# Optimization experiments

Measured on AMD Instinct MI355X. Metric: run time of the kernel, lower is better.

## Reference

```python
import jax, jax.numpy as jnp
import numpy as np

CH = 128
GROUPS = 8
HEADS = 8
HEAD_DIM = CH // HEADS  # 16
EPS = 1e-5


def setup_inputs() -> dict:
    key = jax.random.key(0)
    ks = jax.random.split(key, 5)
    x = jax.random.normal(ks[0], (8, CH, 128, 128), dtype=jnp.float32)
    gn_w = jnp.ones((CH,), dtype=jnp.float32)
    gn_b = jnp.zeros((CH,), dtype=jnp.float32)
    w_in = jax.random.normal(ks[1], (CH, CH), dtype=jnp.float32) * (1.0 / np.sqrt(CH))
    b_in = jax.random.normal(ks[2], (CH,), dtype=jnp.float32) * 0.01
    w_out = jax.random.normal(ks[3], (CH, CH), dtype=jnp.float32) * (1.0 / np.sqrt(CH))
    b_out = jax.random.normal(ks[4], (CH,), dtype=jnp.float32) * 0.01
    return {"x": x, "gn_w": gn_w, "gn_b": gn_b, "w_in": w_in, "b_in": b_in,
            "w_out": w_out, "b_out": b_out}


def _group_norm(x, gamma, beta):
    b, c, H, W = x.shape
    xg = x.reshape(b, GROUPS, c // GROUPS, H, W)
    mean = xg.mean(axis=(2, 3, 4), keepdims=True)
    var = xg.var(axis=(2, 3, 4), keepdims=True)
    xg = (xg - mean) * jax.lax.rsqrt(var + EPS)
    x = xg.reshape(b, c, H, W)
    return x * gamma[None, :, None, None] + beta[None, :, None, None]


def _conv1x1(x, w, bias):
    # w: [out_c, in_c] (1x1 conv == pointwise matmul over channels)
    return jnp.einsum('oc,bchw->bohw', w, x) + bias[None, :, None, None]


def reference(x, gn_w, gn_b, w_in, b_in, w_out, b_out):
    b, c, H, W = x.shape
    h = _group_norm(x, gn_w, gn_b)
    h = _conv1x1(h, w_in, b_in)
    # reshape to [b, heads, head_dim, H*W]; attention over head_dim axis,
    # contracting the spatial axis (d = H*W) as in the original einsums
    hh = h.reshape(b, HEADS, HEAD_DIM, H * W)
    scale = HEAD_DIM ** (-0.5)
    scores = jnp.einsum('bhid,bhjd->bhij', hh, hh) * scale  # [b,heads,hd,hd]
    weights = jax.nn.softmax(scores, axis=-1)
    attn = jnp.einsum('bhij,bhjd->bhid', weights, hh)
    attn = attn.reshape(b, c, H, W)
    h = _conv1x1(attn, w_out, b_out)
    return x + h
```

## Files before the change

kernel.cpp:

```cpp
#include <hip/hip_runtime.h>


#define NPOS 16384
#define PITCH 136

typedef short short8 __attribute__((ext_vector_type(8)));
typedef float f32x4 __attribute__((ext_vector_type(4)));

__device__ __forceinline__ unsigned short f2bf(float f) {
    union { float f; unsigned u; } v; v.f = f;
    unsigned r = (v.u + 0x7fffu + ((v.u >> 16) & 1u)) >> 16;
    return (unsigned short)r;
}

__global__ __launch_bounds__(256) void k_stats(const float* __restrict__ x,
                                               float* __restrict__ stats) {
    const float4* p = (const float4*)(x + (size_t)blockIdx.x * 16384);
    int t = threadIdx.x;
    float s1 = 0.f, s2 = 0.f;
#pragma unroll
    for (int j = 0; j < 16; ++j) {
        float4 v = p[t + j * 256];
        s1 += v.x + v.y + v.z + v.w;
        s2 += v.x * v.x + v.y * v.y + v.z * v.z + v.w * v.w;
    }
    for (int off = 32; off; off >>= 1) {
        s1 += __shfl_down(s1, off);
        s2 += __shfl_down(s2, off);
    }
    __shared__ float r1[4], r2[4];
    int wv = t >> 6;
    if ((t & 63) == 0) { r1[wv] = s1; r2[wv] = s2; }
    __syncthreads();
    if (t == 0) {
        s1 = r1[0] + r1[1] + r1[2] + r1[3];
        s2 = r2[0] + r2[1] + r2[2] + r2[3];
        int bg = blockIdx.x >> 4;
        atomicAdd(&stats[bg * 2 + 0], s1);
        atomicAdd(&stats[bg * 2 + 1], s2);
    }
}

__global__ __launch_bounds__(128) void k_prep(const float* __restrict__ stats,
                                              const float* __restrict__ gn_w,
                                              const float* __restrict__ gn_b,
                                              const float* __restrict__ w_in,
                                              const float* __restrict__ b_in,
                                              float* __restrict__ sA,
                                              float* __restrict__ vA) {
    int b = blockIdx.x, c = threadIdx.x;
    int g = c >> 4;
    float s1 = stats[(b * 8 + g) * 2 + 0];
    float s2 = stats[(b * 8 + g) * 2 + 1];
    const float invN = 1.0f / 262144.0f;
    float mean = s1 * invN;
    float var = s2 * invN - mean * mean;
    float rstd = rsqrtf(var + 1e-5f);
    float s = gn_w[c] * rstd;
    float tt = gn_b[c] - mean * s;
    __shared__ float tl[128];
    tl[c] = tt;
    sA[b * 128 + c] = s;
    __syncthreads();
    float v = b_in[c];
    const float* wr = w_in + c * 128;
#pragma unroll 8
    for (int k = 0; k < 128; ++k) v += wr[k] * tl[k];
    vA[b * 128 + c] = v;
}

__global__ __launch_bounds__(256, 2) void k_gemm1_scores(const float* __restrict__ x,
                                                         const float* __restrict__ w_in,
                                                         const float* __restrict__ sA,
                                                         const float* __restrict__ vA,
                                                         float* __restrict__ Sg) {
    __shared__ unsigned short As[128 * PITCH];
    __shared__ unsigned short Xt[128 * PITCH];
    __shared__ float v_s[128];

    const int t = threadIdx.x;
    const int lane = t & 63, wv = t >> 6;
    const int q = lane >> 4, i16 = lane & 15;
    const int b = blockIdx.x >> 7;
    const int p0 = (blockIdx.x & 127) << 7;

    if (t < 128) v_s[t] = vA[b * 128 + t];

    {
        const float4* w4 = (const float4*)w_in;
        const float4* s4 = (const float4*)(sA + b * 128);
#pragma unroll
        for (int i = 0; i < 16; ++i) {
            int idx = t + i * 256;
            int c = idx >> 5, k4 = idx & 31;
            float4 w = w4[idx];
            float4 s = s4[k4];
            ushort4 o;
            o.x = f2bf(w.x * s.x); o.y = f2bf(w.y * s.y);
            o.z = f2bf(w.z * s.z); o.w = f2bf(w.w * s.w);
            *(ushort4*)&As[c * PITCH + k4 * 4] = o;
        }
    }
    {
        const float* xb = x + (size_t)b * (128 * NPOS) + p0;
#pragma unroll
        for (int i = 0; i < 16; ++i) {
            int p = ((i & 1) << 6) + lane;
            int kq = (wv << 3) + (i >> 1);
            const float* col = xb + (size_t)(kq * 4) * NPOS + p;
            float a0 = col[0];
            float a1 = col[NPOS];
            float a2 = col[2 * NPOS];
            float a3 = col[3 * NPOS];
            ushort4 o; o.x = f2bf(a0); o.y = f2bf(a1); o.z = f2bf(a2); o.w = f2bf(a3);
            *(ushort4*)&Xt[p * PITCH + kq * 4] = o;
        }
    }
    __syncthreads();

    f32x4 acc[2][8];
#pragma unroll
    for (int a = 0; a < 2; ++a)
#pragma unroll
        for (int pt = 0; pt < 8; ++pt) acc[a][pt] = (f32x4){0.f, 0.f, 0.f, 0.f};

#pragma unroll
    for (int ks = 0; ks < 4; ++ks) {
        short8 a0 = *(const short8*)&As[(wv * 32 + i16) * PITCH + ks * 32 + q * 8];
        short8 a1 = *(const short8*)&As[(wv * 32 + 16 + i16) * PITCH + ks * 32 + q * 8];
#pragma unroll
        for (int pt = 0; pt < 8; ++pt) {
            short8 bb = *(const short8*)&Xt[(pt * 16 + i16) * PITCH + ks * 32 + q * 8];
            acc[0][pt] = __builtin_amdgcn_mfma_f32_16x16x32_bf16(a0, bb, acc[0][pt], 0, 0, 0);
            acc[1][pt] = __builtin_amdgcn_mfma_f32_16x16x32_bf16(a1, bb, acc[1][pt], 0, 0, 0);
        }
    }
    __syncthreads();

    unsigned short* Hs = Xt;
#pragma unroll
    for (int a = 0; a < 2; ++a) {
        int cbase = wv * 32 + a * 16 + q * 4;
#pragma unroll
        for (int pt = 0; pt < 8; ++pt) {
            int p = pt * 16 + i16;
#pragma unroll
            for (int r = 0; r < 4; ++r) {
                int c = cbase + r;
                Hs[c * PITCH + p] = f2bf(acc[a][pt][r] + v_s[c]);
            }
        }
    }
    __syncthreads();

#pragma unroll
    for (int hh = 0; hh < 2; ++hh) {
        int h = wv * 2 + hh;
        f32x4 sacc = (f32x4){0.f, 0.f, 0.f, 0.f};
#pragma unroll
        for (int ks = 0; ks < 4; ++ks) {
            short8 f = *(const short8*)&Hs[(h * 16 + i16) * PITCH + ks * 32 + q * 8];
            sacc = __builtin_amdgcn_mfma_f32_16x16x32_bf16(f, f, sacc, 0, 0, 0);
        }
        float* sg = Sg + (b * 8 + h) * 256;
#pragma unroll
        for (int r = 0; r < 4; ++r)
            atomicAdd(&sg[(q * 4 + r) * 16 + i16], sacc[r]);
    }
}

__global__ __launch_bounds__(256) void k_softmax_weff(const float* __restrict__ Sg,
                                                      const float* __restrict__ w_out,
                                                      float* __restrict__ weff) {
    int b = blockIdx.x, t = threadIdx.x;
    __shared__ float W[2048];
    if (t < 128) {
        const float* row = Sg + b * 2048 + t * 16;
        float v[16];
        float m = -1e30f;
#pragma unroll
        for (int j = 0; j < 16; ++j) { v[j] = row[j] * 0.25f; m = fmaxf(m, v[j]); }
        float sum = 0.f;
#pragma unroll
        for (int j = 0; j < 16; ++j) { v[j] = __expf(v[j] - m); sum += v[j]; }
        float inv = 1.0f / sum;
#pragma unroll
        for (int j = 0; j < 16; ++j) W[t * 16 + j] = v[j] * inv;
    }
    __syncthreads();
    float* wo = weff + b * 16384;
#pragma unroll 2
    for (int n = 0; n < 64; ++n) {
        int idx = t + n * 256;
        int c = idx >> 7, k = idx & 127;
        int h = k >> 4, j = k & 15;
        const float* wr = w_out + c * 128 + h * 16;
        const float* Wr = W + h * 256 + j;
        float a = 0.f;
#pragma unroll
        for (int i = 0; i < 16; ++i) a += wr[i] * Wr[i * 16];
        wo[idx] = a;
    }
}

__global__ __launch_bounds__(256, 2) void k_attn_out(const float* __restrict__ x,
                                                     const float* __restrict__ w_in,
                                                     const float* __restrict__ sA,
                                                     const float* __restrict__ vA,
                                                     const float* __restrict__ weff,
                                                     const float* __restrict__ b_out,
                                                     float* __restrict__ out) {
    __shared__ unsigned short As[128 * PITCH];
    __shared__ unsigned short Xt[128 * PITCH];
    __shared__ float v_s[128];
    __shared__ float bo_s[128];

    const int t = threadIdx.x;
    const int lane = t & 63, wv = t >> 6;
    const int q = lane >> 4, i16 = lane & 15;
    const int b = blockIdx.x >> 7;
    const int p0 = (blockIdx.x & 127) << 7;

    if (t < 128) { v_s[t] = vA[b * 128 + t]; bo_s[t] = b_out[t]; }

    const float* xb = x + (size_t)b * (128 * NPOS) + p0;

    {
        const float4* w4 = (const float4*)w_in;
        const float4* s4 = (const float4*)(sA + b * 128);
#pragma unroll
        for (int i = 0; i < 16; ++i) {
            int idx = t + i * 256;
            int c = idx >> 5, k4 = idx & 31;
            float4 w = w4[idx];
            float4 s = s4[k4];
            ushort4 o;
            o.x = f2bf(w.x * s.x); o.y = f2bf(w.y * s.y);
            o.z = f2bf(w.z * s.z); o.w = f2bf(w.w * s.w);
            *(ushort4*)&As[c * PITCH + k4 * 4] = o;
        }
    }
    {
#pragma unroll
        for (int i = 0; i < 16; ++i) {
            int p = ((i & 1) << 6) + lane;
            int kq = (wv << 3) + (i >> 1);
            const float* col = xb + (size_t)(kq * 4) * NPOS + p;
            float a0 = col[0];
            float a1 = col[NPOS];
            float a2 = col[2 * NPOS];
            float a3 = col[3 * NPOS];
            ushort4 o; o.x = f2bf(a0); o.y = f2bf(a1); o.z = f2bf(a2); o.w = f2bf(a3);
            *(ushort4*)&Xt[p * PITCH + kq * 4] = o;
        }
    }
    __syncthreads();

    f32x4 acc[2][8];
#pragma unroll
    for (int a = 0; a < 2; ++a)
#pragma unroll
        for (int pt = 0; pt < 8; ++pt) acc[a][pt] = (f32x4){0.f, 0.f, 0.f, 0.f};

#pragma unroll
    for (int ks = 0; ks < 4; ++ks) {
        short8 a0 = *(const short8*)&As[(wv * 32 + i16) * PITCH + ks * 32 + q * 8];
        short8 a1 = *(const short8*)&As[(wv * 32 + 16 + i16) * PITCH + ks * 32 + q * 8];
#pragma unroll
        for (int pt = 0; pt < 8; ++pt) {
            short8 bb = *(const short8*)&Xt[(pt * 16 + i16) * PITCH + ks * 32 + q * 8];
            acc[0][pt] = __builtin_amdgcn_mfma_f32_16x16x32_bf16(a0, bb, acc[0][pt], 0, 0, 0);
            acc[1][pt] = __builtin_amdgcn_mfma_f32_16x16x32_bf16(a1, bb, acc[1][pt], 0, 0, 0);
        }
    }
    __syncthreads();

#pragma unroll
    for (int a = 0; a < 2; ++a) {
        int cb = wv * 32 + a * 16 + q * 4;
#pragma unroll
        for (int pt = 0; pt < 8; ++pt) {
            int p = pt * 16 + i16;
            ushort4 o;
            o.x = f2bf(acc[a][pt][0] + v_s[cb + 0]);
            o.y = f2bf(acc[a][pt][1] + v_s[cb + 1]);
            o.z = f2bf(acc[a][pt][2] + v_s[cb + 2]);
            o.w = f2bf(acc[a][pt][3] + v_s[cb + 3]);
            *(ushort4*)&Xt[p * PITCH + cb] = o;
        }
    }
    {
        const float4* w4 = (const float4*)(weff + b * 16384);
#pragma unroll
        for (int i = 0; i < 16; ++i) {
            int idx = t + i * 256;
            int c = idx >> 5, k4 = idx & 31;
            float4 w = w4[idx];
            ushort4 o;
            o.x = f2bf(w.x); o.y = f2bf(w.y); o.z = f2bf(w.z); o.w = f2bf(w.w);
            *(ushort4*)&As[c * PITCH + k4 * 4] = o;
        }
    }
    __syncthreads();

#pragma unroll
    for (int a = 0; a < 2; ++a)
#pragma unroll
        for (int pt = 0; pt < 8; ++pt) acc[a][pt] = (f32x4){0.f, 0.f, 0.f, 0.f};

#pragma unroll
    for (int ks = 0; ks < 4; ++ks) {
        short8 a0 = *(const short8*)&As[(wv * 32 + i16) * PITCH + ks * 32 + q * 8];
        short8 a1 = *(const short8*)&As[(wv * 32 + 16 + i16) * PITCH + ks * 32 + q * 8];
#pragma unroll
        for (int pt = 0; pt < 8; ++pt) {
            short8 bb = *(const short8*)&Xt[(pt * 16 + i16) * PITCH + ks * 32 + q * 8];
            acc[0][pt] = __builtin_amdgcn_mfma_f32_16x16x32_bf16(a0, bb, acc[0][pt], 0, 0, 0);
            acc[1][pt] = __builtin_amdgcn_mfma_f32_16x16x32_bf16(a1, bb, acc[1][pt], 0, 0, 0);
        }
    }

    float* ob = out + (size_t)b * (128 * NPOS) + p0;
#pragma unroll
    for (int a = 0; a < 2; ++a) {
        int cb = wv * 32 + a * 16 + q * 4;
#pragma unroll
        for (int pt = 0; pt < 8; ++pt) {
            int p = pt * 16 + i16;
#pragma unroll
            for (int r = 0; r < 4; ++r) {
                int c = cb + r;
                ob[(size_t)c * NPOS + p] = acc[a][pt][r] + bo_s[c] + xb[(size_t)c * NPOS + p];
            }
        }
    }
}

extern "C" void kernel_launch(void* const* d_in, const int* in_sizes, int n_in,
                              void* d_out, int out_size, void* d_ws, size_t ws_size,
                              hipStream_t stream) {
    const float* x    = (const float*)d_in[0];
    const float* gn_w = (const float*)d_in[1];
    const float* gn_b = (const float*)d_in[2];
    const float* w_in = (const float*)d_in[3];
    const float* b_in = (const float*)d_in[4];
    const float* w_out= (const float*)d_in[5];
    const float* b_out= (const float*)d_in[6];
    float* out = (float*)d_out;

    float* ws    = (float*)d_ws;
    float* stats = ws;
    float* Sg    = ws + 128;
    float* sA    = ws + 16512;
    float* vA    = ws + 17536;
    float* weff  = ws + 18560;

    hipMemsetAsync(d_ws, 0, (128 + 16384) * sizeof(float), stream);
    k_stats<<<dim3(1024), dim3(256), 0, stream>>>(x, stats);
    k_prep<<<dim3(8), dim3(128), 0, stream>>>(stats, gn_w, gn_b, w_in, b_in, sA, vA);
    k_gemm1_scores<<<dim3(1024), dim3(256), 0, stream>>>(x, w_in, sA, vA, Sg);
    k_softmax_weff<<<dim3(8), dim3(256), 0, stream>>>(Sg, w_out, weff);
    k_attn_out<<<dim3(1024), dim3(256), 0, stream>>>(x, w_in, sA, vA, weff, b_out, out);
}
```

Measured before the change: 198.9 us.

## Materialize bf16 projected activations and weights to skip recompute in output kernel

Result: no change. 201.8 us (+1.5%).

```diff
diff --git a/kernel.cpp b/kernel.cpp
--- a/kernel.cpp
+++ b/kernel.cpp
@@ -46,8 +46,8 @@
                                               const float* __restrict__ gn_b,
                                               const float* __restrict__ w_in,
                                               const float* __restrict__ b_in,
-                                              float* __restrict__ sA,
-                                              float* __restrict__ vA) {
+                                              float* __restrict__ vA,
+                                              unsigned short* __restrict__ Asb) {
     int b = blockIdx.x, c = threadIdx.x;
     int g = c >> 4;
     float s1 = stats[(b * 8 + g) * 2 + 0];
@@ -58,23 +58,29 @@
     float rstd = rsqrtf(var + 1e-5f);
     float s = gn_w[c] * rstd;
     float tt = gn_b[c] - mean * s;
-    __shared__ float tl[128];
-    tl[c] = tt;
-    sA[b * 128 + c] = s;
+    __shared__ float tl[128], sl[128];
+    tl[c] = tt; sl[c] = s;
     __syncthreads();
     float v = b_in[c];
     const float* wr = w_in + c * 128;
+    unsigned short* ar = Asb + b * 16384 + c * 128;
 #pragma unroll 8
-    for (int k = 0; k < 128; ++k) v += wr[k] * tl[k];
+    for (int k = 0; k < 128; k += 4) {
+        float4 w = *(const float4*)&wr[k];
+        v += w.x * tl[k] + w.y * tl[k + 1] + w.z * tl[k + 2] + w.w * tl[k + 3];
+        ushort4 o;
+        o.x = f2bf(w.x * sl[k]);     o.y = f2bf(w.y * sl[k + 1]);
+        o.z = f2bf(w.z * sl[k + 2]); o.w = f2bf(w.w * sl[k + 3]);
+        *(ushort4*)&ar[k] = o;
+    }
     vA[b * 128 + c] = v;
 }
 
-__global__ __launch_bounds__(256, 2) void k_gemm1_scores(const float* __restrict__ x,
-                                                         const float* __restrict__ w_in,
-                                                         const float* __restrict__ sA,
+__global__ __launch_bounds__(256, 4) void k_gemm1_scores(const float* __restrict__ x,
+                                                         const unsigned short* __restrict__ Asb,
                                                          const float* __restrict__ vA,
+                                                         unsigned short* __restrict__ h1t,
                                                          float* __restrict__ Sg) {
-    __shared__ unsigned short As[128 * PITCH];
     __shared__ unsigned short Xt[128 * PITCH];
     __shared__ float v_s[128];
 
@@ -86,35 +92,18 @@
 
     if (t < 128) v_s[t] = vA[b * 128 + t];
 
-    {
-        const float4* w4 = (const float4*)w_in;
-        const float4* s4 = (const float4*)(sA + b * 128);
-#pragma unroll
-        for (int i = 0; i < 16; ++i) {
-            int idx = t + i * 256;
-            int c = idx >> 5, k4 = idx & 31;
-            float4 w = w4[idx];
-            float4 s = s4[k4];
-            ushort4 o;
-            o.x = f2bf(w.x * s.x); o.y = f2bf(w.y * s.y);
-            o.z = f2bf(w.z * s.z); o.w = f2bf(w.w * s.w);
-            *(ushort4*)&As[c * PITCH + k4 * 4] = o;
-        }
-    }
-    {
-        const float* xb = x + (size_t)b * (128 * NPOS) + p0;
-#pragma unroll
-        for (int i = 0; i < 16; ++i) {
-            int p = ((i & 1) << 6) + lane;
-            int kq = (wv << 3) + (i >> 1);
-            const float* col = xb + (size_t)(kq * 4) * NPOS + p;
-            float a0 = col[0];
-            float a1 = col[NPOS];
-            float a2 = col[2 * NPOS];
-            float a3 = col[3 * NPOS];
-            ushort4 o; o.x = f2bf(a0); o.y = f2bf(a1); o.z = f2bf(a2); o.w = f2bf(a3);
-            *(ushort4*)&Xt[p * PITCH + kq * 4] = o;
-        }
+    const float* xb = x + (size_t)b * (128 * NPOS) + p0;
+#pragma unroll
+    for (int i = 0; i < 16; ++i) {
+        int p = ((i & 1) << 6) + lane;
+        int kq = (wv << 3) + (i >> 1);
+        const float* col = xb + (size_t)(kq * 4) * NPOS + p;
+        float a0 = col[0];
+        float a1 = col[NPOS];
+        float a2 = col[2 * NPOS];
+        float a3 = col[3 * NPOS];
+        ushort4 o; o.x = f2bf(a0); o.y = f2bf(a1); o.z = f2bf(a2); o.w = f2bf(a3);
+        *(ushort4*)&Xt[p * PITCH + kq * 4] = o;
     }
     __syncthreads();
 
@@ -124,10 +113,11 @@
 #pragma unroll
         for (int pt = 0; pt < 8; ++pt) acc[a][pt] = (f32x4){0.f, 0.f, 0.f, 0.f};
 
+    const unsigned short* Ab = Asb + b * 16384;
 #pragma unroll
     for (int ks = 0; ks < 4; ++ks) {
-        short8 a0 = *(const short8*)&As[(wv * 32 + i16) * PITCH + ks * 32 + q * 8];
-        short8 a1 = *(const short8*)&As[(wv * 32 + 16 + i16) * PITCH + ks * 32 + q * 8];
+        short8 a0 = *(const short8*)&Ab[(wv * 32 + i16) * 128 + ks * 32 + q * 8];
+        short8 a1 = *(const short8*)&Ab[(wv * 32 + 16 + i16) * 128 + ks * 32 + q * 8];
 #pragma unroll
         for (int pt = 0; pt < 8; ++pt) {
             short8 bb = *(const short8*)&Xt[(pt * 16 + i16) * PITCH + ks * 32 + q * 8];
@@ -138,143 +128,7 @@
     __syncthreads();
 
     unsigned short* Hs = Xt;
-#pragma unroll
-    for (int a = 0; a < 2; ++a) {
-        int cbase = wv * 32 + a * 16 + q * 4;
-#pragma unroll
-        for (int pt = 0; pt < 8; ++pt) {
-            int p = pt * 16 + i16;
-#pragma unroll
-            for (int r = 0; r < 4; ++r) {
-                int c = cbase + r;
-                Hs[c * PITCH + p] = f2bf(acc[a][pt][r] + v_s[c]);
-            }
-        }
-    }
-    __syncthreads();
-
-#pragma unroll
-    for (int hh = 0; hh < 2; ++hh) {
-        int h = wv * 2 + hh;
-        f32x4 sacc = (f32x4){0.f, 0.f, 0.f, 0.f};
-#pragma unroll
-        for (int ks = 0; ks < 4; ++ks) {
-            short8 f = *(const short8*)&Hs[(h * 16 + i16) * PITCH + ks * 32 + q * 8];
-            sacc = __builtin_amdgcn_mfma_f32_16x16x32_bf16(f, f, sacc, 0, 0, 0);
-        }
-        float* sg = Sg + (b * 8 + h) * 256;
-#pragma unroll
-        for (int r = 0; r < 4; ++r)
-            atomicAdd(&sg[(q * 4 + r) * 16 + i16], sacc[r]);
-    }
-}
-
-__global__ __launch_bounds__(256) void k_softmax_weff(const float* __restrict__ Sg,
-                                                      const float* __restrict__ w_out,
-                                                      float* __restrict__ weff) {
-    int b = blockIdx.x, t = threadIdx.x;
-    __shared__ float W[2048];
-    if (t < 128) {
-        const float* row = Sg + b * 2048 + t * 16;
-        float v[16];
-        float m = -1e30f;
-#pragma unroll
-        for (int j = 0; j < 16; ++j) { v[j] = row[j] * 0.25f; m = fmaxf(m, v[j]); }
-        float sum = 0.f;
-#pragma unroll
-        for (int j = 0; j < 16; ++j) { v[j] = __expf(v[j] - m); sum += v[j]; }
-        float inv = 1.0f / sum;
-#pragma unroll
-        for (int j = 0; j < 16; ++j) W[t * 16 + j] = v[j] * inv;
-    }
-    __syncthreads();
-    float* wo = weff + b * 16384;
-#pragma unroll 2
-    for (int n = 0; n < 64; ++n) {
-        int idx = t + n * 256;
-        int c = idx >> 7, k = idx & 127;
-        int h = k >> 4, j = k & 15;
-        const float* wr = w_out + c * 128 + h * 16;
-        const float* Wr = W + h * 256 + j;
-        float a = 0.f;
-#pragma unroll
-        for (int i = 0; i < 16; ++i) a += wr[i] * Wr[i * 16];
-        wo[idx] = a;
-    }
-}
-
-__global__ __launch_bounds__(256, 2) void k_attn_out(const float* __restrict__ x,
-                                                     const float* __restrict__ w_in,
-                                                     const float* __restrict__ sA,
-                                                     const float* __restrict__ vA,
-                                                     const float* __restrict__ weff,
-                                                     const float* __restrict__ b_out,
-                                                     float* __restrict__ out) {
-    __shared__ unsigned short As[128 * PITCH];
-    __shared__ unsigned short Xt[128 * PITCH];
-    __shared__ float v_s[128];
-    __shared__ float bo_s[128];
-
-    const int t = threadIdx.x;
-    const int lane = t & 63, wv = t >> 6;
-    const int q = lane >> 4, i16 = lane & 15;
-    const int b = blockIdx.x >> 7;
-    const int p0 = (blockIdx.x & 127) << 7;
-
-    if (t < 128) { v_s[t] = vA[b * 128 + t]; bo_s[t] = b_out[t]; }
-
-    const float* xb = x + (size_t)b * (128 * NPOS) + p0;
-
-    {
-        const float4* w4 = (const float4*)w_in;
-        const float4* s4 = (const float4*)(sA + b * 128);
-#pragma unroll
-        for (int i = 0; i < 16; ++i) {
-            int idx = t + i * 256;
-            int c = idx >> 5, k4 = idx & 31;
-            float4 w = w4[idx];
-            float4 s = s4[k4];
-            ushort4 o;
-            o.x = f2bf(w.x * s.x); o.y = f2bf(w.y * s.y);
-            o.z = f2bf(w.z * s.z); o.w = f2bf(w.w * s.w);
-            *(ushort4*)&As[c * PITCH + k4 * 4] = o;
-        }
-    }
-    {
-#pragma unroll
-        for (int i = 0; i < 16; ++i) {
-            int p = ((i & 1) << 6) + lane;
-            int kq = (wv << 3) + (i >> 1);
-            const float* col = xb + (size_t)(kq * 4) * NPOS + p;
-            float a0 = col[0];
-            float a1 = col[NPOS];
-            float a2 = col[2 * NPOS];
-            float a3 = col[3 * NPOS];
-            ushort4 o; o.x = f2bf(a0); o.y = f2bf(a1); o.z = f2bf(a2); o.w = f2bf(a3);
-            *(ushort4*)&Xt[p * PITCH + kq * 4] = o;
-        }
-    }
-    __syncthreads();
-
-    f32x4 acc[2][8];
-#pragma unroll
-    for (int a = 0; a < 2; ++a)
-#pragma unroll
-        for (int pt = 0; pt < 8; ++pt) acc[a][pt] = (f32x4){0.f, 0.f, 0.f, 0.f};
-
-#pragma unroll
-    for (int ks = 0; ks < 4; ++ks) {
-        short8 a0 = *(const short8*)&As[(wv * 32 + i16) * PITCH + ks * 32 + q * 8];
-        short8 a1 = *(const short8*)&As[(wv * 32 + 16 + i16) * PITCH + ks * 32 + q * 8];
-#pragma unroll
-        for (int pt = 0; pt < 8; ++pt) {
-            short8 bb = *(const short8*)&Xt[(pt * 16 + i16) * PITCH + ks * 32 + q * 8];
-            acc[0][pt] = __builtin_amdgcn_mfma_f32_16x16x32_bf16(a0, bb, acc[0][pt], 0, 0, 0);
-            acc[1][pt] = __builtin_amdgcn_mfma_f32_16x16x32_bf16(a1, bb, acc[1][pt], 0, 0, 0);
-        }
-    }
-    __syncthreads();
-
+    unsigned short* hb = h1t + ((size_t)b * NPOS + p0) * 128;
 #pragma unroll
     for (int a = 0; a < 2; ++a) {
         int cb = wv * 32 + a * 16 + q * 4;
@@ -286,40 +140,103 @@
             o.y = f2bf(acc[a][pt][1] + v_s[cb + 1]);
             o.z = f2bf(acc[a][pt][2] + v_s[cb + 2]);
             o.w = f2bf(acc[a][pt][3] + v_s[cb + 3]);
-            *(ushort4*)&Xt[p * PITCH + cb] = o;
-        }
-    }
-    {
-        const float4* w4 = (const float4*)(weff + b * 16384);
-#pragma unroll
-        for (int i = 0; i < 16; ++i) {
-            int idx = t + i * 256;
-            int c = idx >> 5, k4 = idx & 31;
-            float4 w = w4[idx];
-            ushort4 o;
-            o.x = f2bf(w.x); o.y = f2bf(w.y); o.z = f2bf(w.z); o.w = f2bf(w.w);
-            *(ushort4*)&As[c * PITCH + k4 * 4] = o;
-        }
-    }
-    __syncthreads();
-
+            Hs[(cb + 0) * PITCH + p] = o.x;
+            Hs[(cb + 1) * PITCH + p] = o.y;
+            Hs[(cb + 2) * PITCH + p] = o.z;
+            Hs[(cb + 3) * PITCH + p] = o.w;
+            *(ushort4*)&hb[(size_t)p * 128 + cb] = o;
+        }
+    }
+    __syncthreads();
+
+#pragma unroll
+    for (int hh = 0; hh < 2; ++hh) {
+        int h = wv * 2 + hh;
+        f32x4 sacc = (f32x4){0.f, 0.f, 0.f, 0.f};
+#pragma unroll
+        for (int ks = 0; ks < 4; ++ks) {
+            short8 f = *(const short8*)&Hs[(h * 16 + i16) * PITCH + ks * 32 + q * 8];
+            sacc = __builtin_amdgcn_mfma_f32_16x16x32_bf16(f, f, sacc, 0, 0, 0);
+        }
+        float* sg = Sg + (b * 8 + h) * 256;
+#pragma unroll
+        for (int r = 0; r < 4; ++r)
+            atomicAdd(&sg[(q * 4 + r) * 16 + i16], sacc[r]);
+    }
+}
+
+__global__ __launch_bounds__(256) void k_softmax_weff(const float* __restrict__ Sg,
+                                                      const float* __restrict__ w_out,
+                                                      unsigned short* __restrict__ weffb) {
+    int b = blockIdx.x >> 3;
+    int ch = blockIdx.x & 7;
+    int t = threadIdx.x;
+    __shared__ float W[2048];
+    if (t < 128) {
+        const float* row = Sg + b * 2048 + t * 16;
+        float v[16];
+        float m = -1e30f;
+#pragma unroll
+        for (int j = 0; j < 16; ++j) { v[j] = row[j] * 0.25f; m = fmaxf(m, v[j]); }
+        float sum = 0.f;
+#pragma unroll
+        for (int j = 0; j < 16; ++j) { v[j] = __expf(v[j] - m); sum += v[j]; }
+        float inv = 1.0f / sum;
+#pragma unroll
+        for (int j = 0; j < 16; ++j) W[t * 16 + j] = v[j] * inv;
+    }
+    __syncthreads();
+    unsigned short* wo = weffb + b * 16384 + ch * 2048;
+#pragma unroll
+    for (int n = 0; n < 8; ++n) {
+        int idx = t + n * 256;
+        int c = idx >> 7, k = idx & 127;
+        int h = k >> 4, j = k & 15;
+        const float* wr = w_out + (ch * 16 + c) * 128 + h * 16;
+        const float* Wr = W + h * 256 + j;
+        float a = 0.f;
+#pragma unroll
+        for (int i = 0; i < 16; ++i) a += wr[i] * Wr[i * 16];
+        wo[idx] = f2bf(a);
+    }
+}
+
+__global__ __launch_bounds__(256, 4) void k_attn_out(const float* __restrict__ x,
+                                                     const unsigned short* __restrict__ weffb,
+                                                     const unsigned short* __restrict__ h1t,
+                                                     const float* __restrict__ b_out,
+                                                     float* __restrict__ out) {
+    __shared__ float bo_s[128];
+    const int t = threadIdx.x;
+    const int lane = t & 63, wv = t >> 6;
+    const int q = lane >> 4, i16 = lane & 15;
+    const int b = blockIdx.x >> 7;
+    const int p0 = (blockIdx.x & 127) << 7;
+
+    if (t < 128) bo_s[t] = b_out[t];
+    __syncthreads();
+
+    f32x4 acc[2][8];
 #pragma unroll
     for (int a = 0; a < 2; ++a)
 #pragma unroll
         for (int pt = 0; pt < 8; ++pt) acc[a][pt] = (f32x4){0.f, 0.f, 0.f, 0.f};
 
+    const unsigned short* Wb = weffb + b * 16384;
+    const unsigned short* Hb = h1t + ((size_t)b * NPOS + p0) * 128;
 #pragma unroll
     for (int ks = 0; ks < 4; ++ks) {
-        short8 a0 = *(const short8*)&As[(wv * 32 + i16) * PITCH + ks * 32 + q * 8];
-        short8 a1 = *(const short8*)&As[(wv * 32 + 16 + i16) * PITCH + ks * 32 + q * 8];
-#pragma unroll
-        for (int pt = 0; pt < 8; ++pt) {
-            short8 bb = *(const short8*)&Xt[(pt * 16 + i16) * PITCH + ks * 32 + q * 8];
+        short8 a0 = *(const short8*)&Wb[(wv * 32 + i16) * 128 + ks * 32 + q * 8];
+        short8 a1 = *(const short8*)&Wb[(wv * 32 + 16 + i16) * 128 + ks * 32 + q * 8];
+#pragma unroll
+        for (int pt = 0; pt < 8; ++pt) {
+            short8 bb = *(const short8*)&Hb[(size_t)(pt * 16 + i16) * 128 + ks * 32 + q * 8];
             acc[0][pt] = __builtin_amdgcn_mfma_f32_16x16x32_bf16(a0, bb, acc[0][pt], 0, 0, 0);
             acc[1][pt] = __builtin_amdgcn_mfma_f32_16x16x32_bf16(a1, bb, acc[1][pt], 0, 0, 0);
         }
     }
 
+    const float* xb = x + (size_t)b * (128 * NPOS) + p0;
     float* ob = out + (size_t)b * (128 * NPOS) + p0;
 #pragma unroll
     for (int a = 0; a < 2; ++a) {
@@ -348,17 +265,18 @@
     const float* b_out= (const float*)d_in[6];
     float* out = (float*)d_out;
 
-    float* ws    = (float*)d_ws;
-    float* stats = ws;
-    float* Sg    = ws + 128;
-    float* sA    = ws + 16512;
-    float* vA    = ws + 17536;
-    float* weff  = ws + 18560;
-
-    hipMemsetAsync(d_ws, 0, (128 + 16384) * sizeof(float), stream);
+    char* ws = (char*)d_ws;
+    float* stats          = (float*)(ws + 0);
+    float* Sg             = (float*)(ws + 512);
+    float* vA             = (float*)(ws + 66048);
+    unsigned short* Asb   = (unsigned short*)(ws + 70144);
+    unsigned short* weffb = (unsigned short*)(ws + 332288);
+    unsigned short* h1t   = (unsigned short*)(ws + 594432);
+
+    hipMemsetAsync(d_ws, 0, 66048, stream);
     k_stats<<<dim3(1024), dim3(256), 0, stream>>>(x, stats);
-    k_prep<<<dim3(8), dim3(128), 0, stream>>>(stats, gn_w, gn_b, w_in, b_in, sA, vA);
-    k_gemm1_scores<<<dim3(1024), dim3(256), 0, stream>>>(x, w_in, sA, vA, Sg);
-    k_softmax_weff<<<dim3(8), dim3(256), 0, stream>>>(Sg, w_out, weff);
-    k_attn_out<<<dim3(1024), dim3(256), 0, stream>>>(x, w_in, sA, vA, weff, b_out, out);
-}
+    k_prep<<<dim3(8), dim3(128), 0, stream>>>(stats, gn_w, gn_b, w_in, b_in, vA, Asb);
+    k_gemm1_scores<<<dim3(1024), dim3(256), 0, stream>>>(x, Asb, vA, h1t, Sg);
+    k_softmax_weff<<<dim3(64), dim3(256), 0, stream>>>(Sg, w_out, weffb);
+    k_attn_out<<<dim3(1024), dim3(256), 0, stream>>>(x, weffb, h1t, b_out, out);
+}
```
